# Performance work log

Measured on AMD Instinct MI355X. Metric: run time of the kernel, lower is better.

Reference implementation:

```python
import jax, jax.numpy as jnp
import numpy as np

B, S, D = 128, 512, 1024          # batch, ctx seqlen, model dim
GEN_V, INP_V, OUT_V = 50000, 30000, 50257  # gen vocab, input vocab, output vocab


def setup_inputs() -> dict:
    key = jax.random.key(0)
    ks = jax.random.split(key, 7)
    x = jax.random.normal(ks[0], (B, D), jnp.float32)
    alphas = jax.random.uniform(ks[1], (B, S), jnp.float32)
    alphas = alphas / alphas.sum(-1, keepdims=True)  # normalized attention probs
    ctx_inp = jax.random.randint(ks[2], (B, S), 0, INP_V)
    gen_to_out = jax.random.randint(ks[3], (GEN_V,), 0, OUT_V)
    inp_to_out = jax.random.randint(ks[4], (INP_V,), 0, OUT_V)
    W_gate = jax.random.normal(ks[5], (D, 1), jnp.float32) * 0.02
    b_gate = jnp.zeros((1,), jnp.float32)
    W_gen = jax.random.normal(ks[6], (D, GEN_V), jnp.float32) * 0.02
    b_gen = jnp.zeros((GEN_V,), jnp.float32)
    return {"x": x, "alphas": alphas, "W_gate": W_gate, "b_gate": b_gate,
            "W_gen": W_gen, "b_gen": b_gen, "ctx_inp": ctx_inp,
            "gen_to_out": gen_to_out, "inp_to_out": inp_to_out}


def reference(x, alphas, W_gate, b_gate, W_gen, b_gen, ctx_inp, gen_to_out, inp_to_out):
    # gate: probability of generating vs pointing  [B,1]
    interp = jax.nn.sigmoid(x @ W_gate + b_gate)
    # generation distribution over gen vocab       [B,GEN_V]
    gen_probs = jax.nn.softmax(x @ W_gen + b_gen, axis=-1)
    # scatter_add gen probs into output vocab (same index map for all rows)
    out_gen = jax.ops.segment_sum(gen_probs.T, gen_to_out, num_segments=OUT_V).T  # [B,OUT_V]
    # scatter_add pointer probs into output vocab (per-row indices)
    ctx_out = inp_to_out[ctx_inp]  # [B,S]
    rows = jnp.arange(x.shape[0])[:, None]
    out_ptr = jnp.zeros((x.shape[0], OUT_V), x.dtype).at[rows, ctx_out].add(alphas)
    # interpolated mixture
    return interp * out_gen + (1.0 - interp) * out_ptr
```

## Files before the change

kernel.cpp:

```cpp
#include <hip/hip_runtime.h>
#include <hip/hip_bf16.h>
#include <cstdint>
#include <cstddef>

#define B_ 128
#define D_ 1024
#define GEN_V_ 50000
#define OUT_V_ 50257
#define S_ 512
#define NCH_ 99

#define NTILE 64
#define NBLK 782
#define BK 64
#define LD 72

typedef __attribute__((ext_vector_type(8))) short bf16x8;
typedef __attribute__((ext_vector_type(8))) unsigned short u16x8;
typedef __attribute__((ext_vector_type(4))) float f32x4;

__device__ __forceinline__ unsigned short f2bf(float f) {
  unsigned u = __float_as_uint(f);
  u += 0x7fffu + ((u >> 16) & 1u);
  return (unsigned short)(u >> 16);
}

__global__ void gate_kernel(const float* __restrict__ x, const float* __restrict__ Wg,
                            const float* __restrict__ bg, float* __restrict__ interp) {
  int b = blockIdx.x;
  int t = threadIdx.x;
  const float4* xr = (const float4*)(x + (size_t)b * D_);
  const float4* wr = (const float4*)Wg;
  float s = 0.f;
  for (int i = t; i < D_ / 4; i += 256) {
    float4 xv = xr[i], wv = wr[i];
    s += xv.x * wv.x + xv.y * wv.y + xv.z * wv.z + xv.w * wv.w;
  }
  for (int o = 32; o > 0; o >>= 1) s += __shfl_down(s, o);
  __shared__ float red[4];
  int lane = t & 63, w = t >> 6;
  if (lane == 0) red[w] = s;
  __syncthreads();
  if (t == 0) {
    float tot = red[0] + red[1] + red[2] + red[3] + bg[0];
    interp[b] = 1.f / (1.f + __expf(-tot));
  }
}

__global__ __launch_bounds__(512, 4) void gemm_kernel(
    const float* __restrict__ x, const float* __restrict__ W,
    const float* __restrict__ bgen, float* __restrict__ elog,
    float* __restrict__ rowpart) {
  __shared__ unsigned short sA[B_][LD];
  __shared__ unsigned short sB[NTILE][LD];
  __shared__ float srow[B_];
  int tid = threadIdx.x;
  int lane = tid & 63;
  int wv = tid >> 6;
  int wm = wv & 1;
  int wn = wv >> 1;
  int nbase = blockIdx.x * NTILE;
  int l15 = lane & 15;
  int quad = lane >> 4;
  int koff0 = quad * 8;

  f32x4 acc[4];
#pragma unroll
  for (int i = 0; i < 4; i++) acc[i] = (f32x4){0.f, 0.f, 0.f, 0.f};

  int bn = lane;
  int kc = wv;
  bool colv = (nbase + bn) < GEN_V_;
  const float* Wcol = W + (size_t)kc * 8 * GEN_V_ + nbase + bn;

  const float4* xg = (const float4*)x;

  for (int k0 = 0; k0 < D_; k0 += BK) {
    int kb4 = k0 >> 2;
#pragma unroll
    for (int i = 0; i < 4; i++) {
      int q = tid + i * 512;
      int m = q >> 4, c4 = q & 15;
      float4 v = xg[(size_t)m * (D_ / 4) + kb4 + c4];
      ushort4 h;
      h.x = f2bf(v.x); h.y = f2bf(v.y); h.z = f2bf(v.z); h.w = f2bf(v.w);
      *(ushort4*)&sA[m][c4 * 4] = h;
    }
    {
      const float* Wp = Wcol + (size_t)k0 * GEN_V_;
      u16x8 hh;
#pragma unroll
      for (int j = 0; j < 8; j++) {
        float w = colv ? Wp[(size_t)j * GEN_V_] : 0.f;
        hh[j] = f2bf(w);
      }
      *(u16x8*)&sB[bn][kc * 8] = hh;
    }
    __syncthreads();
#pragma unroll
    for (int ks = 0; ks < BK; ks += 32) {
      int koff = ks + koff0;
      bf16x8 bfr = *(const bf16x8*)&sB[wn * 16 + l15][koff];
      bf16x8 af[4];
#pragma unroll
      for (int mt = 0; mt < 4; mt++)
        af[mt] = *(const bf16x8*)&sA[wm * 64 + mt * 16 + l15][koff];
#pragma unroll
      for (int mt = 0; mt < 4; mt++)
        acc[mt] = __builtin_amdgcn_mfma_f32_16x16x32_bf16(af[mt], bfr, acc[mt], 0, 0, 0);
    }
    __syncthreads();
  }

  if (tid < B_) srow[tid] = 0.f;
  __syncthreads();
  int cg = nbase + wn * 16 + l15;
  bool cv = cg < GEN_V_;
  float bgv = cv ? bgen[cg] : 0.f;
  int rquad = quad * 4;
#pragma unroll
  for (int mt = 0; mt < 4; mt++) {
    int rb = wm * 64 + mt * 16 + rquad;
#pragma unroll
    for (int r = 0; r < 4; r++) {
      float e = __expf(acc[mt][r] + bgv);
      float contrib = cv ? e : 0.f;
      if (cv) elog[(size_t)(rb + r) * GEN_V_ + cg] = e;
#pragma unroll
      for (int o = 1; o < 16; o <<= 1) contrib += __shfl_xor(contrib, o);
      if (l15 == 0) atomicAdd(&srow[rb + r], contrib);
    }
  }
  __syncthreads();
  if (tid < B_) rowpart[(size_t)tid * NBLK + blockIdx.x] = srow[tid];
}

__global__ void rowsum_kernel(const float* __restrict__ rowpart, const float* __restrict__ interp,
                              float* __restrict__ rowscale) {
  int b = blockIdx.x, t = threadIdx.x;
  const float* rp = rowpart + (size_t)b * NBLK;
  float s = 0.f;
  for (int i = t; i < NBLK; i += 256) s += rp[i];
  for (int o = 32; o > 0; o >>= 1) s += __shfl_down(s, o);
  __shared__ float red[4];
  int lane = t & 63, w = t >> 6;
  if (lane == 0) red[w] = s;
  __syncthreads();
  if (t == 0) rowscale[b] = interp[b] / (red[0] + red[1] + red[2] + red[3]);
}

__global__ void hist_kernel(const int* __restrict__ g2o, int* __restrict__ counts) {
  int v = blockIdx.x * 256 + threadIdx.x;
  if (v < GEN_V_) atomicAdd(&counts[g2o[v]], 1);
}

__global__ void chunkred_kernel(const int* __restrict__ counts, int* __restrict__ blocksums) {
  int c = blockIdx.x, t = threadIdx.x;
  int o0 = c * 512 + t;
  int s = 0;
  if (o0 < OUT_V_) s += counts[o0];
  if (o0 + 256 < OUT_V_) s += counts[o0 + 256];
  for (int o = 32; o > 0; o >>= 1) s += __shfl_down(s, o);
  __shared__ int red[4];
  int lane = t & 63, w = t >> 6;
  if (lane == 0) red[w] = s;
  __syncthreads();
  if (t == 0) blocksums[c] = red[0] + red[1] + red[2] + red[3];
}

__global__ void scanbase_kernel(int* __restrict__ blocksums, int* __restrict__ offsets) {
  __shared__ int sh[128];
  int t = threadIdx.x;
  sh[t] = (t < NCH_) ? blocksums[t] : 0;
  __syncthreads();
#pragma unroll
  for (int d = 1; d < 128; d <<= 1) {
    int v = (t >= d) ? sh[t - d] : 0;
    __syncthreads();
    sh[t] += v;
    __syncthreads();
  }
  if (t < NCH_) blocksums[t] = (t == 0) ? 0 : sh[t - 1];
  if (t == 0) offsets[OUT_V_] = GEN_V_;
}

__global__ void scanchunk_kernel(const int* __restrict__ counts, const int* __restrict__ blocksums,
                                 int* __restrict__ offsets, int* __restrict__ cursor) {
  __shared__ int sh[512];
  int c = blockIdx.x, t = threadIdx.x;
  int o = c * 512 + t;
  int own = (o < OUT_V_) ? counts[o] : 0;
  sh[t] = own;
  __syncthreads();
#pragma unroll
  for (int d = 1; d < 512; d <<= 1) {
    int v = (t >= d) ? sh[t - d] : 0;
    __syncthreads();
    sh[t] += v;
    __syncthreads();
  }
  if (o < OUT_V_) {
    int excl = sh[t] - own + blocksums[c];
    offsets[o] = excl;
    cursor[o] = excl;
  }
}

__global__ void permscat_kernel(const int* __restrict__ g2o, int* __restrict__ cursor,
                                int* __restrict__ perm) {
  int v = blockIdx.x * 256 + threadIdx.x;
  if (v < GEN_V_) {
    int pos = atomicAdd(&cursor[g2o[v]], 1);
    perm[pos] = v;
  }
}

__global__ void gather_gen_kernel(const float* __restrict__ elog, const int* __restrict__ perm,
                                  const int* __restrict__ offsets,
                                  const float* __restrict__ rowscale, float* __restrict__ out) {
  int o = blockIdx.x * 256 + threadIdx.x;
  int b = blockIdx.y;
  if (o < OUT_V_) {
    int s0 = offsets[o], s1 = offsets[o + 1];
    float sc = rowscale[b];
    const float* lrow = elog + (size_t)b * GEN_V_;
    float s = 0.f;
    for (int j = s0; j < s1; j++) s += lrow[perm[j]];
    out[(size_t)b * OUT_V_ + o] = s * sc;
  }
}

__global__ void scatter_ptr_kernel(const float* __restrict__ alphas, const int* __restrict__ ctx,
                                   const int* __restrict__ i2o, const float* __restrict__ interp,
                                   float* __restrict__ out) {
  int b = blockIdx.x, s = threadIdx.x;
  float w = 1.f - interp[b];
  int o = i2o[ctx[b * S_ + s]];
  atomicAdd(&out[(size_t)b * OUT_V_ + o], w * alphas[b * S_ + s]);
}

extern "C" void kernel_launch(void* const* d_in, const int* in_sizes, int n_in,
                              void* d_out, int out_size, void* d_ws, size_t ws_size,
                              hipStream_t stream) {
  const float* x      = (const float*)d_in[0];
  const float* alphas = (const float*)d_in[1];
  const float* Wg     = (const float*)d_in[2];
  const float* bg     = (const float*)d_in[3];
  const float* Wgen   = (const float*)d_in[4];
  const float* bgen   = (const float*)d_in[5];
  const int*   ctx    = (const int*)d_in[6];
  const int*   g2o    = (const int*)d_in[7];
  const int*   i2o    = (const int*)d_in[8];
  float* out = (float*)d_out;

  float* elog      = (float*)d_ws;
  float* interp    = elog + (size_t)B_ * GEN_V_;
  float* rowscale  = interp + B_;
  float* rowpart   = rowscale + B_;
  int*   counts    = (int*)(rowpart + (size_t)B_ * NBLK);
  int*   offsets   = counts + OUT_V_;
  int*   cursor    = offsets + (OUT_V_ + 1);
  int*   perm      = cursor + OUT_V_;
  int*   blocksums = perm + GEN_V_;

  hipMemsetAsync(counts, 0, OUT_V_ * sizeof(int), stream);

  gate_kernel<<<B_, 256, 0, stream>>>(x, Wg, bg, interp);
  gemm_kernel<<<NBLK, 512, 0, stream>>>(x, Wgen, bgen, elog, rowpart);
  rowsum_kernel<<<B_, 256, 0, stream>>>(rowpart, interp, rowscale);

  hist_kernel<<<(GEN_V_ + 255) / 256, 256, 0, stream>>>(g2o, counts);
  chunkred_kernel<<<NCH_, 256, 0, stream>>>(counts, blocksums);
  scanbase_kernel<<<1, 128, 0, stream>>>(blocksums, offsets);
  scanchunk_kernel<<<NCH_, 512, 0, stream>>>(counts, blocksums, offsets, cursor);
  permscat_kernel<<<(GEN_V_ + 255) / 256, 256, 0, stream>>>(g2o, cursor, perm);

  gather_gen_kernel<<<dim3((OUT_V_ + 255) / 256, B_), 256, 0, stream>>>(
      elog, perm, offsets, rowscale, out);
  scatter_ptr_kernel<<<B_, S_, 0, stream>>>(alphas, ctx, i2o, interp, out);
}
```

Baseline: 409.2 us.

## Fuse gen-vocab scatter into GEMM epilogue via global atomics, drop CSR build

The GEMM epilogue now atomically adds exp(logit) straight into the zeroed output at the mapped output-vocab index, instead of writing an exp-logit buffer. This removes the histogram/scan/permutation pipeline and the gather kernel. A separate pass then scales each output row by interp/rowsum before the pointer scatter. It trades the elog write and gather reads for a full output memset, 6.4M global float atomics and an extra read-write pass over the output. Atomic accumulation order also makes the result nondeterministic.

```diff
diff --git a/kernel.cpp b/kernel.cpp
--- a/kernel.cpp
+++ b/kernel.cpp
@@ -8,7 +8,6 @@
 #define GEN_V_ 50000
 #define OUT_V_ 50257
 #define S_ 512
-#define NCH_ 99
 
 #define NTILE 64
 #define NBLK 782
@@ -47,10 +46,10 @@
   }
 }
 
-__global__ __launch_bounds__(512, 4) void gemm_kernel(
+__global__ __launch_bounds__(512, 4) void gemm_scatter_kernel(
     const float* __restrict__ x, const float* __restrict__ W,
-    const float* __restrict__ bgen, float* __restrict__ elog,
-    float* __restrict__ rowpart) {
+    const float* __restrict__ bgen, const int* __restrict__ g2o,
+    float* __restrict__ out, float* __restrict__ rowpart) {
   __shared__ unsigned short sA[B_][LD];
   __shared__ unsigned short sB[NTILE][LD];
   __shared__ float srow[B_];
@@ -117,6 +116,7 @@
   int cg = nbase + wn * 16 + l15;
   bool cv = cg < GEN_V_;
   float bgv = cv ? bgen[cg] : 0.f;
+  int og = cv ? g2o[cg] : 0;
   int rquad = quad * 4;
 #pragma unroll
   for (int mt = 0; mt < 4; mt++) {
@@ -125,7 +125,7 @@
     for (int r = 0; r < 4; r++) {
       float e = __expf(acc[mt][r] + bgv);
       float contrib = cv ? e : 0.f;
-      if (cv) elog[(size_t)(rb + r) * GEN_V_ + cg] = e;
+      if (cv) atomicAdd(&out[(size_t)(rb + r) * OUT_V_ + og], e);
 #pragma unroll
       for (int o = 1; o < 16; o <<= 1) contrib += __shfl_xor(contrib, o);
       if (l15 == 0) atomicAdd(&srow[rb + r], contrib);
@@ -149,84 +149,24 @@
   if (t == 0) rowscale[b] = interp[b] / (red[0] + red[1] + red[2] + red[3]);
 }
 
-__global__ void hist_kernel(const int* __restrict__ g2o, int* __restrict__ counts) {
-  int v = blockIdx.x * 256 + threadIdx.x;
-  if (v < GEN_V_) atomicAdd(&counts[g2o[v]], 1);
-}
-
-__global__ void chunkred_kernel(const int* __restrict__ counts, int* __restrict__ blocksums) {
-  int c = blockIdx.x, t = threadIdx.x;
-  int o0 = c * 512 + t;
-  int s = 0;
-  if (o0 < OUT_V_) s += counts[o0];
-  if (o0 + 256 < OUT_V_) s += counts[o0 + 256];
-  for (int o = 32; o > 0; o >>= 1) s += __shfl_down(s, o);
-  __shared__ int red[4];
-  int lane = t & 63, w = t >> 6;
-  if (lane == 0) red[w] = s;
-  __syncthreads();
-  if (t == 0) blocksums[c] = red[0] + red[1] + red[2] + red[3];
-}
-
-__global__ void scanbase_kernel(int* __restrict__ blocksums, int* __restrict__ offsets) {
-  __shared__ int sh[128];
-  int t = threadIdx.x;
-  sh[t] = (t < NCH_) ? blocksums[t] : 0;
-  __syncthreads();
-#pragma unroll
-  for (int d = 1; d < 128; d <<= 1) {
-    int v = (t >= d) ? sh[t - d] : 0;
-    __syncthreads();
-    sh[t] += v;
-    __syncthreads();
-  }
-  if (t < NCH_) blocksums[t] = (t == 0) ? 0 : sh[t - 1];
-  if (t == 0) offsets[OUT_V_] = GEN_V_;
-}
-
-__global__ void scanchunk_kernel(const int* __restrict__ counts, const int* __restrict__ blocksums,
-                                 int* __restrict__ offsets, int* __restrict__ cursor) {
-  __shared__ int sh[512];
-  int c = blockIdx.x, t = threadIdx.x;
-  int o = c * 512 + t;
-  int own = (o < OUT_V_) ? counts[o] : 0;
-  sh[t] = own;
-  __syncthreads();
-#pragma unroll
-  for (int d = 1; d < 512; d <<= 1) {
-    int v = (t >= d) ? sh[t - d] : 0;
-    __syncthreads();
-    sh[t] += v;
-    __syncthreads();
-  }
-  if (o < OUT_V_) {
-    int excl = sh[t] - own + blocksums[c];
-    offsets[o] = excl;
-    cursor[o] = excl;
-  }
-}
-
-__global__ void permscat_kernel(const int* __restrict__ g2o, int* __restrict__ cursor,
-                                int* __restrict__ perm) {
-  int v = blockIdx.x * 256 + threadIdx.x;
-  if (v < GEN_V_) {
-    int pos = atomicAdd(&cursor[g2o[v]], 1);
-    perm[pos] = v;
-  }
-}
-
-__global__ void gather_gen_kernel(const float* __restrict__ elog, const int* __restrict__ perm,
-                                  const int* __restrict__ offsets,
-                                  const float* __restrict__ rowscale, float* __restrict__ out) {
-  int o = blockIdx.x * 256 + threadIdx.x;
-  int b = blockIdx.y;
-  if (o < OUT_V_) {
-    int s0 = offsets[o], s1 = offsets[o + 1];
-    float sc = rowscale[b];
-    const float* lrow = elog + (size_t)b * GEN_V_;
-    float s = 0.f;
-    for (int j = s0; j < s1; j++) s += lrow[perm[j]];
-    out[(size_t)b * OUT_V_ + o] = s * sc;
+#define NFLT4 ((B_ * OUT_V_) / 4)
+__global__ void scale_kernel(float* __restrict__ out, const float* __restrict__ rowscale) {
+  unsigned i4 = blockIdx.x * 256u + threadIdx.x;
+  if (i4 < (unsigned)NFLT4) {
+    float4 v = ((float4*)out)[i4];
+    unsigned e = i4 * 4u;
+    unsigned b0 = e / OUT_V_;
+    unsigned b3 = (e + 3u) / OUT_V_;
+    if (b0 == b3) {
+      float sc = rowscale[b0];
+      v.x *= sc; v.y *= sc; v.z *= sc; v.w *= sc;
+    } else {
+      v.x *= rowscale[e / OUT_V_];
+      v.y *= rowscale[(e + 1u) / OUT_V_];
+      v.z *= rowscale[(e + 2u) / OUT_V_];
+      v.w *= rowscale[(e + 3u) / OUT_V_];
+    }
+    ((float4*)out)[i4] = v;
   }
 }
 
@@ -253,29 +193,15 @@
   const int*   i2o    = (const int*)d_in[8];
   float* out = (float*)d_out;
 
-  float* elog      = (float*)d_ws;
-  float* interp    = elog + (size_t)B_ * GEN_V_;
-  float* rowscale  = interp + B_;
-  float* rowpart   = rowscale + B_;
-  int*   counts    = (int*)(rowpart + (size_t)B_ * NBLK);
-  int*   offsets   = counts + OUT_V_;
-  int*   cursor    = offsets + (OUT_V_ + 1);
-  int*   perm      = cursor + OUT_V_;
-  int*   blocksums = perm + GEN_V_;
-
-  hipMemsetAsync(counts, 0, OUT_V_ * sizeof(int), stream);
+  float* interp   = (float*)d_ws;
+  float* rowscale = interp + B_;
+  float* rowpart  = rowscale + B_;
+
+  hipMemsetAsync(out, 0, (size_t)B_ * OUT_V_ * sizeof(float), stream);
 
   gate_kernel<<<B_, 256, 0, stream>>>(x, Wg, bg, interp);
-  gemm_kernel<<<NBLK, 512, 0, stream>>>(x, Wgen, bgen, elog, rowpart);
+  gemm_scatter_kernel<<<NBLK, 512, 0, stream>>>(x, Wgen, bgen, g2o, out, rowpart);
   rowsum_kernel<<<B_, 256, 0, stream>>>(rowpart, interp, rowscale);
-
-  hist_kernel<<<(GEN_V_ + 255) / 256, 256, 0, stream>>>(g2o, counts);
-  chunkred_kernel<<<NCH_, 256, 0, stream>>>(counts, blocksums);
-  scanbase_kernel<<<1, 128, 0, stream>>>(blocksums, offsets);
-  scanchunk_kernel<<<NCH_, 512, 0, stream>>>(counts, blocksums, offsets, cursor);
-  permscat_kernel<<<(GEN_V_ + 255) / 256, 256, 0, stream>>>(g2o, cursor, perm);
-
-  gather_gen_kernel<<<dim3((OUT_V_ + 255) / 256, B_), 256, 0, stream>>>(
-      elog, perm, offsets, rowscale, out);
+  scale_kernel<<<(NFLT4 + 255) / 256, 256, 0, stream>>>(out, rowscale);
   scatter_ptr_kernel<<<B_, S_, 0, stream>>>(alphas, ctx, i2o, interp, out);
 }
```

New measurement: 633.9 us. 54.9% more time.
